# Optimization experiments

Hardware: AMD Instinct MI355X
Metric: run time of the kernel (lower is better)

Reference implementation:

```python
import jax, jax.numpy as jnp
import numpy as np

B, S, D = 8, 4096, 1024
G, V = 2, 320
TAU = 1.0
EPS = 1e-7


def setup_inputs() -> dict:
    key = jax.random.key(0)
    k_x, k_w, k_cb, k_u = jax.random.split(key, 4)
    x = jax.random.normal(k_x, (B, S, D), dtype=jnp.float32)
    W = jax.random.normal(k_w, (D, G * V), dtype=jnp.float32) * (1.0 / np.sqrt(D))
    b = jnp.zeros((G * V,), dtype=jnp.float32)
    # nn.init.uniform_ -> U(0,1); codebooks viewed as [G, V, D//G]
    codebooks = jax.random.uniform(k_cb, (G, V, D // G), dtype=jnp.float32)
    # standard Gumbel(0,1) noise, one per logit: shape [B*S*G, V]
    u = jax.random.uniform(k_u, (B * S * G, V), dtype=jnp.float32,
                           minval=1e-6, maxval=1.0 - 1e-6)
    gumbel = -jnp.log(-jnp.log(u))
    return {"x": x, "W": W, "b": b, "codebooks": codebooks, "gumbel": gumbel}


def reference(x, W, b, codebooks, gumbel):
    Bx, Sx, Dx = x.shape
    Gx, Vx, _ = codebooks.shape
    N = Bx * Sx
    # logit projection: [B,S,D] @ [D, G*V] -> flatten to [N*G, V]
    logits = (jnp.einsum('bsd,de->bse', x, W) + b).reshape(N * Gx, Vx)
    # gumbel-softmax, hard=True with straight-through estimator
    y_soft = jax.nn.softmax((logits + gumbel) / TAU, axis=-1)
    idx = jnp.argmax(y_soft, axis=-1)
    y_hard = jax.nn.one_hot(idx, Vx, dtype=y_soft.dtype)
    one_hot_st = y_hard + y_soft - jax.lax.stop_gradient(y_soft)  # fwd == y_hard
    # codebook lookup via (mostly one-hot) contraction: [N,G,V] x [G,V,d] -> [N,G,d]
    q = jnp.einsum('ngv,gvd->ngd', one_hot_st.reshape(N, Gx, Vx), codebooks)
    quantized = q.reshape(Bx, Sx, Dx)
    # perplexity from clean (non-gumbel) softmax probs
    probs = jax.nn.softmax(logits.reshape(N, Gx, Vx), axis=-1)
    avg_probs = probs.mean(axis=0)  # [G, V]
    perplexity = jnp.exp(-jnp.sum(avg_probs * jnp.log(avg_probs + EPS), axis=-1)).mean()
    return (quantized, perplexity)
```

## Files before the change

kernel.cpp:

```cpp
#include <hip/hip_runtime.h>
#include <hip/hip_bf16.h>
#include <math.h>

#define NROWS 32768
#define DD    1024
#define EE    640
#define VV    320
#define BM    64
#define KT    32
#define CTN   40

typedef __attribute__((ext_vector_type(8))) short short8;
typedef __attribute__((ext_vector_type(4))) short short4v;
typedef __attribute__((ext_vector_type(4))) float float4v;

static __device__ __forceinline__ unsigned short f2bf(float f) {
    unsigned int u = __float_as_uint(f);
    return (unsigned short)((u + 0x7fffu + ((u >> 16) & 1u)) >> 16);
}

static __device__ __forceinline__ void gload_lds16(const void* g, void* l) {
    __builtin_amdgcn_global_load_lds(
        (const __attribute__((address_space(1))) unsigned int*)g,
        (__attribute__((address_space(3))) unsigned int*)l, 16, 0, 0);
}

__global__ void pack_w(const float* __restrict__ W, unsigned short* __restrict__ bp)
{
    const int t = threadIdx.x;
    const int tile = blockIdx.x * 4 + (t >> 6);
    const int lane = t & 63;
    const int kt = tile / CTN, ct = tile % CTN;
    const int k0 = kt * 32 + (lane >> 4) * 8;
    const int col = ct * 16 + (lane & 15);
    unsigned short v1[8];
    #pragma unroll
    for (int e = 0; e < 8; ++e)
        v1[e] = f2bf(W[(size_t)(k0 + e) * EE + col]);
    *(short8*)(bp + ((size_t)tile * 64 + lane) * 8) = *(const short8*)v1;
}

__global__ __launch_bounds__(512, 4) void fused_mfma(
    const float* __restrict__ x, const unsigned short* __restrict__ bp,
    const float* __restrict__ bias, const float* __restrict__ cb,
    const float* __restrict__ gum, float* __restrict__ out,
    float* __restrict__ probs_acc)
{
    __shared__ unsigned short Bs[32 * EE];
    __shared__ unsigned short As[BM * 32];
    __shared__ float probs_blk[EE];
    __shared__ float pmax[8][BM];
    __shared__ float psum[8][BM];
    __shared__ int   pidx[8][BM];
    __shared__ int   fidx[BM][2];
    __shared__ float finv[BM][2];

    const int t    = threadIdx.x;
    const int lane = t & 63;
    const int cg   = t >> 6;
    const int n0   = blockIdx.x * BM;

    float4v acc[4][5];
    #pragma unroll
    for (int rf = 0; rf < 4; ++rf)
        #pragma unroll
        for (int ct = 0; ct < 5; ++ct)
            acc[rf][ct] = (float4v)0.f;

    const int r0 = t >> 3, kq0 = t & 7;
    const int abase = (r0 >> 4)*512 + ((r0 & 15) + ((kq0 >> 1) << 4))*8 + ((kq0 & 1) << 2);
    const float* xr = x + (size_t)(n0 + r0) * DD + kq0 * 4;

    auto writeA = [&](float4 v) {
        short4v s1;
        s1[0] = (short)f2bf(v.x); s1[1] = (short)f2bf(v.y);
        s1[2] = (short)f2bf(v.z); s1[3] = (short)f2bf(v.w);
        *(short4v*)&As[abase] = s1;
    };
    auto stageB = [&](int kt) {
        const unsigned short* src = bp + (size_t)kt * (32 * EE);
        #pragma unroll
        for (int s = 0; s < 5; ++s) {
            const int q = s * 512 + t;
            gload_lds16(src + (size_t)q * 8, &Bs[q * 8]);
        }
    };

    float4 pA = *(const float4*)(xr);
    stageB(0);
    __syncthreads();
    writeA(pA);
    __syncthreads();

    for (int kt = 0; kt < KT; ++kt) {
        const bool more = (kt + 1 < KT);
        if (more) pA = *(const float4*)(xr + (kt + 1) * 32);

        short8 af[4];
        #pragma unroll
        for (int rf = 0; rf < 4; ++rf)
            af[rf] = *(const short8*)&As[rf*512 + lane*8];
        #pragma unroll
        for (int ct = 0; ct < 5; ++ct) {
            short8 bf = *(const short8*)&Bs[((cg*5 + ct)*64 + lane)*8];
            #pragma unroll
            for (int rf = 0; rf < 4; ++rf)
                acc[rf][ct] = __builtin_amdgcn_mfma_f32_16x16x32_bf16(af[rf], bf, acc[rf][ct], 0, 0, 0);
        }
        __syncthreads();
        if (more) {
            stageB(kt + 1);
            writeA(pA);
        }
        __syncthreads();
    }

    {
        float bv[5];
        #pragma unroll
        for (int ct = 0; ct < 5; ++ct) bv[ct] = bias[cg*80 + ct*16 + (lane & 15)];
        #pragma unroll
        for (int rf = 0; rf < 4; ++rf)
            #pragma unroll
            for (int ct = 0; ct < 5; ++ct) {
                acc[rf][ct][0] += bv[ct]; acc[rf][ct][1] += bv[ct];
                acc[rf][ct][2] += bv[ct]; acc[rf][ct][3] += bv[ct];
            }
    }

    const int g = cg >> 2;
    const int goff0 = (cg & 3)*80 + (lane & 15);
    #pragma unroll
    for (int rf = 0; rf < 4; ++rf) {
        #pragma unroll
        for (int r = 0; r < 4; ++r) {
            const int rowA = rf*16 + ((lane >> 4) << 2) + r;
            const float* grow = gum + ((size_t)(n0 + rowA)*2 + g)*VV + goff0;
            float m1 = -1e30f; int bi = 0; float es = 0.f;
            #pragma unroll
            for (int ct = 0; ct < 5; ++ct) {
                float z  = acc[rf][ct][r];
                float zg = z + grow[ct*16];
                if (zg > m1) { m1 = zg; bi = goff0 + ct*16; }
                es += __expf(z);
            }
            #pragma unroll
            for (int off = 1; off < 16; off <<= 1) {
                float om = __shfl_xor(m1, off);
                int   ob = __shfl_xor(bi, off);
                if (om > m1 || (om == m1 && ob < bi)) { m1 = om; bi = ob; }
                es += __shfl_xor(es, off);
            }
            if ((lane & 15) == 0) {
                pmax[cg][rowA] = m1; pidx[cg][rowA] = bi; psum[cg][rowA] = es;
            }
        }
    }
    for (int c = t; c < EE; c += 512) probs_blk[c] = 0.f;
    __syncthreads();

    if (t < 128) {
        const int row = t & 63, gg = t >> 6;
        float m1 = -1e30f; int bi = 0x7fffffff; float s = 0.f;
        #pragma unroll
        for (int c = 0; c < 4; ++c) {
            const float om = pmax[gg*4 + c][row];
            const int   ob = pidx[gg*4 + c][row];
            if (om > m1 || (om == m1 && ob < bi)) { m1 = om; bi = ob; }
            s += psum[gg*4 + c][row];
        }
        fidx[row][gg] = bi;
        finv[row][gg] = 1.f / s;
    }
    __syncthreads();

    float pacc[5];
    #pragma unroll
    for (int ct = 0; ct < 5; ++ct) pacc[ct] = 0.f;
    #pragma unroll
    for (int rf = 0; rf < 4; ++rf) {
        #pragma unroll
        for (int r = 0; r < 4; ++r) {
            const int rowA = rf*16 + ((lane >> 4) << 2) + r;
            const float inv = finv[rowA][g];
            #pragma unroll
            for (int ct = 0; ct < 5; ++ct)
                pacc[ct] += __expf(acc[rf][ct][r]) * inv;
        }
    }
    #pragma unroll
    for (int off = 16; off < 64; off <<= 1)
        #pragma unroll
        for (int ct = 0; ct < 5; ++ct)
            pacc[ct] += __shfl_xor(pacc[ct], off);
    if (lane < 16) {
        #pragma unroll
        for (int ct = 0; ct < 5; ++ct)
            atomicAdd(&probs_blk[cg*80 + ct*16 + lane], pacc[ct]);
    }
    __syncthreads();

    for (int c = t; c < EE; c += 512)
        atomicAdd(&probs_acc[c], probs_blk[c]);

    for (int i = t; i < BM*256; i += 512) {
        const int row = i >> 8, f4 = i & 255;
        const int gg  = f4 >> 7;
        const int idx = fidx[row][gg];
        const float4 v = *(const float4*)&cb[((size_t)gg*VV + idx)*512 + (size_t)(f4 & 127)*4];
        *(float4*)&out[(size_t)(n0 + row)*DD + (size_t)f4*4] = v;
    }
}

__global__ void perp_kernel(const float* __restrict__ probs_acc,
                            float* __restrict__ outp)
{
    __shared__ float s0[4], s1[4];
    int t = threadIdx.x;
    float p0 = 0.f, p1 = 0.f;
    for (int c = t; c < EE; c += 256) {
        float a = probs_acc[c] * (1.0f / NROWS);
        float v = a * logf(a + 1e-7f);
        if (c < VV) p0 += v; else p1 += v;
    }
    #pragma unroll
    for (int off = 1; off < 64; off <<= 1) {
        p0 += __shfl_xor(p0, off);
        p1 += __shfl_xor(p1, off);
    }
    if ((t & 63) == 0) { s0[t >> 6] = p0; s1[t >> 6] = p1; }
    __syncthreads();
    if (t == 0) {
        float a0 = s0[0] + s0[1] + s0[2] + s0[3];
        float a1 = s1[0] + s1[1] + s1[2] + s1[3];
        outp[0] = 0.5f * (expf(-a0) + expf(-a1));
    }
}

extern "C" void kernel_launch(void* const* d_in, const int* in_sizes, int n_in,
                              void* d_out, int out_size, void* d_ws, size_t ws_size,
                              hipStream_t stream)
{
    const float* x   = (const float*)d_in[0];
    const float* W   = (const float*)d_in[1];
    const float* b   = (const float*)d_in[2];
    const float* cb  = (const float*)d_in[3];
    const float* gum = (const float*)d_in[4];
    float* out = (float*)d_out;

    unsigned short* bp = (unsigned short*)d_ws;
    float* probs_acc = (float*)((char*)d_ws + (size_t)DD*EE*2);

    hipMemsetAsync(probs_acc, 0, EE * sizeof(float), stream);
    pack_w<<<320, 256, 0, stream>>>(W, bp);
    fused_mfma<<<NROWS / BM, 512, 0, stream>>>(x, bp, b, cb, gum, out, probs_acc);
    perp_kernel<<<1, 256, 0, stream>>>(probs_acc, out + (out_size - 1));
}
```

Before: 131.0 us.

## Double-buffer LDS tiles and double row tile to 1024-thread blocks

The row tile per block grows from 64 to 128, so each W tile staged into LDS now serves twice as many rows, using 16 waves arranged as 2 row groups by 8 column groups. The A and B LDS tiles are double-buffered: the next K-step's global-to-LDS copy is issued before the current MFMA work, which drops one barrier per iteration. The cost is roughly 100 KB of LDS per block, so only one block fits per CU. The launch bound of (1024, 4) may also squeeze the register budget hard enough to cause spills of the 80-float accumulator array.

```diff
diff --git a/kernel.cpp b/kernel.cpp
--- a/kernel.cpp
+++ b/kernel.cpp
@@ -6,7 +6,7 @@
 #define DD    1024
 #define EE    640
 #define VV    320
-#define BM    64
+#define BM    128
 #define KT    32
 #define CTN   40
 
@@ -40,14 +40,14 @@
     *(short8*)(bp + ((size_t)tile * 64 + lane) * 8) = *(const short8*)v1;
 }
 
-__global__ __launch_bounds__(512, 4) void fused_mfma(
+__global__ __launch_bounds__(1024, 4) void fused_mfma(
     const float* __restrict__ x, const unsigned short* __restrict__ bp,
     const float* __restrict__ bias, const float* __restrict__ cb,
     const float* __restrict__ gum, float* __restrict__ out,
     float* __restrict__ probs_acc)
 {
-    __shared__ unsigned short Bs[32 * EE];
-    __shared__ unsigned short As[BM * 32];
+    __shared__ unsigned short Bs[2][32 * EE];
+    __shared__ unsigned short As[2][BM * 32];
     __shared__ float probs_blk[EE];
     __shared__ float pmax[8][BM];
     __shared__ float psum[8][BM];
@@ -57,7 +57,9 @@
 
     const int t    = threadIdx.x;
     const int lane = t & 63;
-    const int cg   = t >> 6;
+    const int w    = t >> 6;
+    const int rg   = w >> 3;
+    const int cg   = w & 7;
     const int n0   = blockIdx.x * BM;
 
     float4v acc[4][5];
@@ -71,48 +73,47 @@
     const int abase = (r0 >> 4)*512 + ((r0 & 15) + ((kq0 >> 1) << 4))*8 + ((kq0 & 1) << 2);
     const float* xr = x + (size_t)(n0 + r0) * DD + kq0 * 4;
 
-    auto writeA = [&](float4 v) {
+    auto writeA = [&](int bb, float4 v) {
         short4v s1;
         s1[0] = (short)f2bf(v.x); s1[1] = (short)f2bf(v.y);
         s1[2] = (short)f2bf(v.z); s1[3] = (short)f2bf(v.w);
-        *(short4v*)&As[abase] = s1;
+        *(short4v*)&As[bb][abase] = s1;
     };
-    auto stageB = [&](int kt) {
+    auto stageB = [&](int bb, int kt) {
         const unsigned short* src = bp + (size_t)kt * (32 * EE);
-        #pragma unroll
-        for (int s = 0; s < 5; ++s) {
-            const int q = s * 512 + t;
-            gload_lds16(src + (size_t)q * 8, &Bs[q * 8]);
-        }
+        gload_lds16(src + (size_t)t * 8,          &Bs[bb][t * 8]);
+        gload_lds16(src + (size_t)(t + 1024) * 8, &Bs[bb][(t + 1024) * 8]);
+        if (t < 512)
+            gload_lds16(src + (size_t)(t + 2048) * 8, &Bs[bb][(t + 2048) * 8]);
     };
 
     float4 pA = *(const float4*)(xr);
-    stageB(0);
-    __syncthreads();
-    writeA(pA);
-    __syncthreads();
-
+    stageB(0, 0);
+    __syncthreads();
+    writeA(0, pA);
+    __syncthreads();
+
+    int cur = 0;
     for (int kt = 0; kt < KT; ++kt) {
         const bool more = (kt + 1 < KT);
-        if (more) pA = *(const float4*)(xr + (kt + 1) * 32);
-
+        if (more) {
+            stageB(cur ^ 1, kt + 1);
+            pA = *(const float4*)(xr + (kt + 1) * 32);
+        }
         short8 af[4];
         #pragma unroll
         for (int rf = 0; rf < 4; ++rf)
-            af[rf] = *(const short8*)&As[rf*512 + lane*8];
+            af[rf] = *(const short8*)&As[cur][(rg*4 + rf)*512 + lane*8];
         #pragma unroll
         for (int ct = 0; ct < 5; ++ct) {
-            short8 bf = *(const short8*)&Bs[((cg*5 + ct)*64 + lane)*8];
+            short8 bf = *(const short8*)&Bs[cur][((cg*5 + ct)*64 + lane)*8];
             #pragma unroll
             for (int rf = 0; rf < 4; ++rf)
                 acc[rf][ct] = __builtin_amdgcn_mfma_f32_16x16x32_bf16(af[rf], bf, acc[rf][ct], 0, 0, 0);
         }
+        if (more) writeA(cur ^ 1, pA);
         __syncthreads();
-        if (more) {
-            stageB(kt + 1);
-            writeA(pA);
-        }
-        __syncthreads();
+        cur ^= 1;
     }
 
     {
@@ -134,7 +135,7 @@
     for (int rf = 0; rf < 4; ++rf) {
         #pragma unroll
         for (int r = 0; r < 4; ++r) {
-            const int rowA = rf*16 + ((lane >> 4) << 2) + r;
+            const int rowA = rg*64 + rf*16 + ((lane >> 4) << 2) + r;
             const float* grow = gum + ((size_t)(n0 + rowA)*2 + g)*VV + goff0;
             float m1 = -1e30f; int bi = 0; float es = 0.f;
             #pragma unroll
@@ -156,11 +157,11 @@
             }
         }
     }
-    for (int c = t; c < EE; c += 512) probs_blk[c] = 0.f;
-    __syncthreads();
-
-    if (t < 128) {
-        const int row = t & 63, gg = t >> 6;
+    for (int c = t; c < EE; c += 1024) probs_blk[c] = 0.f;
+    __syncthreads();
+
+    if (t < 256) {
+        const int row = t & 127, gg = t >> 7;
         float m1 = -1e30f; int bi = 0x7fffffff; float s = 0.f;
         #pragma unroll
         for (int c = 0; c < 4; ++c) {
@@ -181,7 +182,7 @@
     for (int rf = 0; rf < 4; ++rf) {
         #pragma unroll
         for (int r = 0; r < 4; ++r) {
-            const int rowA = rf*16 + ((lane >> 4) << 2) + r;
+            const int rowA = rg*64 + rf*16 + ((lane >> 4) << 2) + r;
             const float inv = finv[rowA][g];
             #pragma unroll
             for (int ct = 0; ct < 5; ++ct)
@@ -200,10 +201,10 @@
     }
     __syncthreads();
 
-    for (int c = t; c < EE; c += 512)
+    for (int c = t; c < EE; c += 1024)
         atomicAdd(&probs_acc[c], probs_blk[c]);
 
-    for (int i = t; i < BM*256; i += 512) {
+    for (int i = t; i < BM*256; i += 1024) {
         const int row = i >> 8, f4 = i & 255;
         const int gg  = f4 >> 7;
         const int idx = fidx[row][gg];
@@ -253,6 +254,6 @@
 
     hipMemsetAsync(probs_acc, 0, EE * sizeof(float), stream);
     pack_w<<<320, 256, 0, stream>>>(W, bp);
-    fused_mfma<<<NROWS / BM, 512, 0, stream>>>(x, bp, b, cb, gum, out, probs_acc);
+    fused_mfma<<<NROWS / BM, 1024, 0, stream>>>(x, bp, b, cb, gum, out, probs_acc);
     perp_kernel<<<1, 256, 0, stream>>>(probs_acc, out + (out_size - 1));
 }
```

New measurement: 130.6 us. Within noise of the previous version (-0.3%).

## Split fused kernel into GEMM writing bf16 logits and separate epilogue kernel

Applied to the files above, without the earlier changes.

Unfuses the projection from the softmax/argmax/codebook epilogue. The GEMM now stores bias-added logits as bf16 to workspace, double-buffers B tiles in LDS, and loads A directly from global with in-register bf16 conversion instead of staging through LDS. A new epilogue kernel processes 16 rows per block using LDS copies of logits and gumbel noise. Probability sums are accumulated into 8 replicated buffers to reduce atomic contention. This adds a logits round trip through memory and bf16 rounding of logits before argmax, and every wave now loads the same A data redundantly.

```diff
diff --git a/kernel.cpp b/kernel.cpp
--- a/kernel.cpp
+++ b/kernel.cpp
@@ -6,19 +6,28 @@
 #define DD    1024
 #define EE    640
 #define VV    320
-#define BM    64
 #define KT    32
 #define CTN   40
 
 typedef __attribute__((ext_vector_type(8))) short short8;
-typedef __attribute__((ext_vector_type(4))) short short4v;
 typedef __attribute__((ext_vector_type(4))) float float4v;
 
 static __device__ __forceinline__ unsigned short f2bf(float f) {
     unsigned int u = __float_as_uint(f);
     return (unsigned short)((u + 0x7fffu + ((u >> 16) & 1u)) >> 16);
 }
-
+static __device__ __forceinline__ float bf2f(unsigned short h) {
+    return __uint_as_float(((unsigned int)h) << 16);
+}
+static __device__ __forceinline__ short8 cvt8(float4 a, float4 b) {
+    float2 f0 = {a.x, a.y}, f1 = {a.z, a.w}, f2 = {b.x, b.y}, f3 = {b.z, b.w};
+    union { __hip_bfloat162 h[4]; short8 s; } u;
+    u.h[0] = __float22bfloat162_rn(f0);
+    u.h[1] = __float22bfloat162_rn(f1);
+    u.h[2] = __float22bfloat162_rn(f2);
+    u.h[3] = __float22bfloat162_rn(f3);
+    return u.s;
+}
 static __device__ __forceinline__ void gload_lds16(const void* g, void* l) {
     __builtin_amdgcn_global_load_lds(
         (const __attribute__((address_space(1))) unsigned int*)g,
@@ -40,25 +49,16 @@
     *(short8*)(bp + ((size_t)tile * 64 + lane) * 8) = *(const short8*)v1;
 }
 
-__global__ __launch_bounds__(512, 4) void fused_mfma(
+__global__ __launch_bounds__(512, 4) void gemm_z2(
     const float* __restrict__ x, const unsigned short* __restrict__ bp,
-    const float* __restrict__ bias, const float* __restrict__ cb,
-    const float* __restrict__ gum, float* __restrict__ out,
-    float* __restrict__ probs_acc)
-{
-    __shared__ unsigned short Bs[32 * EE];
-    __shared__ unsigned short As[BM * 32];
-    __shared__ float probs_blk[EE];
-    __shared__ float pmax[8][BM];
-    __shared__ float psum[8][BM];
-    __shared__ int   pidx[8][BM];
-    __shared__ int   fidx[BM][2];
-    __shared__ float finv[BM][2];
+    const float* __restrict__ bias, unsigned short* __restrict__ z)
+{
+    __shared__ unsigned short Bs[2][32 * EE];
 
     const int t    = threadIdx.x;
     const int lane = t & 63;
     const int cg   = t >> 6;
-    const int n0   = blockIdx.x * BM;
+    const int n0   = blockIdx.x * 64;
 
     float4v acc[4][5];
     #pragma unroll
@@ -67,159 +67,147 @@
         for (int ct = 0; ct < 5; ++ct)
             acc[rf][ct] = (float4v)0.f;
 
-    const int r0 = t >> 3, kq0 = t & 7;
-    const int abase = (r0 >> 4)*512 + ((r0 & 15) + ((kq0 >> 1) << 4))*8 + ((kq0 & 1) << 2);
-    const float* xr = x + (size_t)(n0 + r0) * DD + kq0 * 4;
-
-    auto writeA = [&](float4 v) {
-        short4v s1;
-        s1[0] = (short)f2bf(v.x); s1[1] = (short)f2bf(v.y);
-        s1[2] = (short)f2bf(v.z); s1[3] = (short)f2bf(v.w);
-        *(short4v*)&As[abase] = s1;
-    };
-    auto stageB = [&](int kt) {
+    const float* xl = x + (size_t)(n0 + (lane & 15)) * DD + (lane >> 4) * 8;
+
+    auto stageB = [&](int bb, int kt) {
         const unsigned short* src = bp + (size_t)kt * (32 * EE);
         #pragma unroll
         for (int s = 0; s < 5; ++s) {
             const int q = s * 512 + t;
-            gload_lds16(src + (size_t)q * 8, &Bs[q * 8]);
+            gload_lds16(src + (size_t)q * 8, &Bs[bb][q * 8]);
         }
     };
 
-    float4 pA = *(const float4*)(xr);
-    stageB(0);
-    __syncthreads();
-    writeA(pA);
-    __syncthreads();
-
+    stageB(0, 0);
     for (int kt = 0; kt < KT; ++kt) {
-        const bool more = (kt + 1 < KT);
-        if (more) pA = *(const float4*)(xr + (kt + 1) * 32);
+        asm volatile("s_waitcnt vmcnt(0)" ::: "memory");
+        __builtin_amdgcn_s_barrier();
+        __builtin_amdgcn_sched_barrier(0);
+        if (kt + 1 < KT) stageB((kt + 1) & 1, kt + 1);
+        __builtin_amdgcn_sched_barrier(0);
 
         short8 af[4];
         #pragma unroll
-        for (int rf = 0; rf < 4; ++rf)
-            af[rf] = *(const short8*)&As[rf*512 + lane*8];
+        for (int rf = 0; rf < 4; ++rf) {
+            float4 a0 = *(const float4*)(xl + (size_t)rf * 16 * DD + kt * 32);
+            float4 a1 = *(const float4*)(xl + (size_t)rf * 16 * DD + kt * 32 + 4);
+            af[rf] = cvt8(a0, a1);
+        }
         #pragma unroll
         for (int ct = 0; ct < 5; ++ct) {
-            short8 bf = *(const short8*)&Bs[((cg*5 + ct)*64 + lane)*8];
+            short8 bf = *(const short8*)&Bs[kt & 1][((cg*5 + ct)*64 + lane)*8];
             #pragma unroll
             for (int rf = 0; rf < 4; ++rf)
                 acc[rf][ct] = __builtin_amdgcn_mfma_f32_16x16x32_bf16(af[rf], bf, acc[rf][ct], 0, 0, 0);
         }
-        __syncthreads();
-        if (more) {
-            stageB(kt + 1);
-            writeA(pA);
-        }
-        __syncthreads();
-    }
+    }
+
+    float bv[5];
+    const int cb0 = cg * 80 + (lane & 15);
+    #pragma unroll
+    for (int ct = 0; ct < 5; ++ct) bv[ct] = bias[cb0 + ct*16];
+    #pragma unroll
+    for (int rf = 0; rf < 4; ++rf) {
+        #pragma unroll
+        for (int r = 0; r < 4; ++r) {
+            const size_t n = (size_t)(n0 + rf*16 + ((lane >> 4) << 2) + r);
+            #pragma unroll
+            for (int ct = 0; ct < 5; ++ct)
+                z[n*EE + cb0 + ct*16] = f2bf(acc[rf][ct][r] + bv[ct]);
+        }
+    }
+}
+
+__global__ __launch_bounds__(512, 2) void epi2(
+    const unsigned short* __restrict__ z, const float* __restrict__ gum,
+    const float* __restrict__ cb, float* __restrict__ out,
+    float* __restrict__ probs_rep)
+{
+    __shared__ unsigned short zs[16 * EE];
+    __shared__ float          gs[16 * EE];
+    __shared__ float inv[16][2];
+    __shared__ int   sidx[16][2];
+
+    const int t = threadIdx.x;
+    const size_t r0 = (size_t)blockIdx.x * 16;
 
     {
-        float bv[5];
-        #pragma unroll
-        for (int ct = 0; ct < 5; ++ct) bv[ct] = bias[cg*80 + ct*16 + (lane & 15)];
-        #pragma unroll
-        for (int rf = 0; rf < 4; ++rf)
-            #pragma unroll
-            for (int ct = 0; ct < 5; ++ct) {
-                acc[rf][ct][0] += bv[ct]; acc[rf][ct][1] += bv[ct];
-                acc[rf][ct][2] += bv[ct]; acc[rf][ct][3] += bv[ct];
-            }
-    }
-
-    const int g = cg >> 2;
-    const int goff0 = (cg & 3)*80 + (lane & 15);
-    #pragma unroll
-    for (int rf = 0; rf < 4; ++rf) {
-        #pragma unroll
-        for (int r = 0; r < 4; ++r) {
-            const int rowA = rf*16 + ((lane >> 4) << 2) + r;
-            const float* grow = gum + ((size_t)(n0 + rowA)*2 + g)*VV + goff0;
-            float m1 = -1e30f; int bi = 0; float es = 0.f;
-            #pragma unroll
-            for (int ct = 0; ct < 5; ++ct) {
-                float z  = acc[rf][ct][r];
-                float zg = z + grow[ct*16];
-                if (zg > m1) { m1 = zg; bi = goff0 + ct*16; }
-                es += __expf(z);
-            }
-            #pragma unroll
-            for (int off = 1; off < 16; off <<= 1) {
-                float om = __shfl_xor(m1, off);
-                int   ob = __shfl_xor(bi, off);
-                if (om > m1 || (om == m1 && ob < bi)) { m1 = om; bi = ob; }
-                es += __shfl_xor(es, off);
-            }
-            if ((lane & 15) == 0) {
-                pmax[cg][rowA] = m1; pidx[cg][rowA] = bi; psum[cg][rowA] = es;
-            }
-        }
-    }
-    for (int c = t; c < EE; c += 512) probs_blk[c] = 0.f;
+        const uint4* src = (const uint4*)(z + r0 * EE);
+        uint4* dst = (uint4*)zs;
+        dst[t]       = src[t];
+        dst[t + 512] = src[t + 512];
+        if (t < 256) dst[t + 1024] = src[t + 1024];
+        const uint4* gsrc = (const uint4*)(gum + r0 * 2 * VV);
+        uint4* gdst = (uint4*)gs;
+        #pragma unroll
+        for (int s = 0; s < 5; ++s) gdst[t + s*512] = gsrc[t + s*512];
+    }
     __syncthreads();
 
-    if (t < 128) {
-        const int row = t & 63, gg = t >> 6;
-        float m1 = -1e30f; int bi = 0x7fffffff; float s = 0.f;
-        #pragma unroll
-        for (int c = 0; c < 4; ++c) {
-            const float om = pmax[gg*4 + c][row];
-            const int   ob = pidx[gg*4 + c][row];
+    {
+        const int row = t >> 5, j = t & 31, g = j >> 4, vb = (j & 15) * 20;
+        const unsigned short* zrow = &zs[row * EE + g * VV + vb];
+        const float* grow = &gs[row * EE + g * VV + vb];
+        float m1 = -1e30f; int bi = 0; float es = 0.f;
+        #pragma unroll
+        for (int k = 0; k < 20; ++k) {
+            const float zj = bf2f(zrow[k]);
+            const float zg = zj + grow[k];
+            if (zg > m1) { m1 = zg; bi = vb + k; }
+            es += __expf(zj);
+        }
+        #pragma unroll
+        for (int off = 1; off < 16; off <<= 1) {
+            float om = __shfl_xor(m1, off);
+            int   ob = __shfl_xor(bi, off);
             if (om > m1 || (om == m1 && ob < bi)) { m1 = om; bi = ob; }
-            s += psum[gg*4 + c][row];
-        }
-        fidx[row][gg] = bi;
-        finv[row][gg] = 1.f / s;
+            es += __shfl_xor(es, off);
+        }
+        if ((j & 15) == 0) { sidx[row][g] = bi; inv[row][g] = 1.f / es; }
     }
     __syncthreads();
 
-    float pacc[5];
-    #pragma unroll
-    for (int ct = 0; ct < 5; ++ct) pacc[ct] = 0.f;
-    #pragma unroll
-    for (int rf = 0; rf < 4; ++rf) {
-        #pragma unroll
-        for (int r = 0; r < 4; ++r) {
-            const int rowA = rf*16 + ((lane >> 4) << 2) + r;
-            const float inv = finv[rowA][g];
-            #pragma unroll
-            for (int ct = 0; ct < 5; ++ct)
-                pacc[ct] += __expf(acc[rf][ct][r]) * inv;
-        }
-    }
-    #pragma unroll
-    for (int off = 16; off < 64; off <<= 1)
-        #pragma unroll
-        for (int ct = 0; ct < 5; ++ct)
-            pacc[ct] += __shfl_xor(pacc[ct], off);
-    if (lane < 16) {
-        #pragma unroll
-        for (int ct = 0; ct < 5; ++ct)
-            atomicAdd(&probs_blk[cg*80 + ct*16 + lane], pacc[ct]);
-    }
-    __syncthreads();
-
-    for (int c = t; c < EE; c += 512)
-        atomicAdd(&probs_acc[c], probs_blk[c]);
-
-    for (int i = t; i < BM*256; i += 512) {
-        const int row = i >> 8, f4 = i & 255;
-        const int gg  = f4 >> 7;
-        const int idx = fidx[row][gg];
+    {
+        const int rep = blockIdx.x & 7;
+        int c = t;
+        {
+            const int gg = (c >= VV);
+            float s = 0.f;
+            #pragma unroll
+            for (int rr = 0; rr < 16; ++rr)
+                s += __expf(bf2f(zs[rr * EE + c])) * inv[rr][gg];
+            atomicAdd(&probs_rep[rep * EE + c], s);
+        }
+        if (t < 128) {
+            c = 512 + t;
+            float s = 0.f;
+            #pragma unroll
+            for (int rr = 0; rr < 16; ++rr)
+                s += __expf(bf2f(zs[rr * EE + c])) * inv[rr][1];
+            atomicAdd(&probs_rep[rep * EE + c], s);
+        }
+    }
+
+    for (int i = t; i < 16 * 256; i += 512) {
+        const int rr = i >> 8, f4 = i & 255;
+        const int gg = f4 >> 7;
+        const int idx = sidx[rr][gg];
         const float4 v = *(const float4*)&cb[((size_t)gg*VV + idx)*512 + (size_t)(f4 & 127)*4];
-        *(float4*)&out[(size_t)(n0 + row)*DD + (size_t)f4*4] = v;
-    }
-}
-
-__global__ void perp_kernel(const float* __restrict__ probs_acc,
-                            float* __restrict__ outp)
+        *(float4*)&out[(r0 + rr)*DD + (size_t)f4*4] = v;
+    }
+}
+
+__global__ void perp8_kernel(const float* __restrict__ probs_rep,
+                             float* __restrict__ outp)
 {
     __shared__ float s0[4], s1[4];
     int t = threadIdx.x;
     float p0 = 0.f, p1 = 0.f;
     for (int c = t; c < EE; c += 256) {
-        float a = probs_acc[c] * (1.0f / NROWS);
+        float a = 0.f;
+        #pragma unroll
+        for (int rp = 0; rp < 8; ++rp) a += probs_rep[rp*EE + c];
+        a *= (1.0f / NROWS);
         float v = a * logf(a + 1e-7f);
         if (c < VV) p0 += v; else p1 += v;
     }
@@ -248,11 +236,16 @@
     const float* gum = (const float*)d_in[4];
     float* out = (float*)d_out;
 
-    unsigned short* bp = (unsigned short*)d_ws;
-    float* probs_acc = (float*)((char*)d_ws + (size_t)DD*EE*2);
-
-    hipMemsetAsync(probs_acc, 0, EE * sizeof(float), stream);
+    char* wsp = (char*)d_ws;
+    unsigned short* bp = (unsigned short*)wsp;
+    const size_t bp_b = (size_t)DD*EE*2;
+    float* probs_rep = (float*)(wsp + bp_b);
+    const size_t pr_b = 8*EE*sizeof(float);
+    unsigned short* z = (unsigned short*)(wsp + bp_b + pr_b);
+
+    hipMemsetAsync(probs_rep, 0, pr_b, stream);
     pack_w<<<320, 256, 0, stream>>>(W, bp);
-    fused_mfma<<<NROWS / BM, 512, 0, stream>>>(x, bp, b, cb, gum, out, probs_acc);
-    perp_kernel<<<1, 256, 0, stream>>>(probs_acc, out + (out_size - 1));
-}
+    gemm_z2<<<NROWS / 64, 512, 0, stream>>>(x, bp, b, z);
+    epi2<<<NROWS / 16, 512, 0, stream>>>(z, gum, cb, out, probs_rep);
+    perp8_kernel<<<1, 256, 0, stream>>>(probs_rep, out + (out_size - 1));
+}
```

Result: slower. 230.6 us (+76.0%).

## Switch logit GEMM to FP8 MFMA with double-buffered LDS staging

Applied to the files above, without the earlier changes.

Converts both the x tiles and the packed W (pre-scaled by 16) to FP8 and uses the fp8 16x16x32 MFMA, rescaling the accumulators before adding the bias. LDS buffers for A and B are double-buffered so the next tile's load is issued before the current MFMAs, which drops one barrier per k-step. The probability accumulation is spread across 8 replicated global buffers to reduce atomic contention, and the final kernel sums the replicas. FP8 precision can change argmax indices on near-ties and alter the perplexity, which risks accuracy.

```diff
diff --git a/kernel.cpp b/kernel.cpp
--- a/kernel.cpp
+++ b/kernel.cpp
@@ -10,14 +10,8 @@
 #define KT    32
 #define CTN   40
 
-typedef __attribute__((ext_vector_type(8))) short short8;
-typedef __attribute__((ext_vector_type(4))) short short4v;
 typedef __attribute__((ext_vector_type(4))) float float4v;
-
-static __device__ __forceinline__ unsigned short f2bf(float f) {
-    unsigned int u = __float_as_uint(f);
-    return (unsigned short)((u + 0x7fffu + ((u >> 16) & 1u)) >> 16);
-}
+typedef long long i64t;
 
 static __device__ __forceinline__ void gload_lds16(const void* g, void* l) {
     __builtin_amdgcn_global_load_lds(
@@ -25,7 +19,7 @@
         (__attribute__((address_space(3))) unsigned int*)l, 16, 0, 0);
 }
 
-__global__ void pack_w(const float* __restrict__ W, unsigned short* __restrict__ bp)
+__global__ void pack_w8(const float* __restrict__ W, unsigned char* __restrict__ bp)
 {
     const int t = threadIdx.x;
     const int tile = blockIdx.x * 4 + (t >> 6);
@@ -33,21 +27,27 @@
     const int kt = tile / CTN, ct = tile % CTN;
     const int k0 = kt * 32 + (lane >> 4) * 8;
     const int col = ct * 16 + (lane & 15);
-    unsigned short v1[8];
+    float v[8];
     #pragma unroll
     for (int e = 0; e < 8; ++e)
-        v1[e] = f2bf(W[(size_t)(k0 + e) * EE + col]);
-    *(short8*)(bp + ((size_t)tile * 64 + lane) * 8) = *(const short8*)v1;
-}
-
-__global__ __launch_bounds__(512, 4) void fused_mfma(
-    const float* __restrict__ x, const unsigned short* __restrict__ bp,
+        v[e] = 16.0f * W[(size_t)(k0 + e) * EE + col];
+    int lo = 0, hi = 0;
+    lo = __builtin_amdgcn_cvt_pk_fp8_f32(v[0], v[1], lo, false);
+    lo = __builtin_amdgcn_cvt_pk_fp8_f32(v[2], v[3], lo, true);
+    hi = __builtin_amdgcn_cvt_pk_fp8_f32(v[4], v[5], hi, false);
+    hi = __builtin_amdgcn_cvt_pk_fp8_f32(v[6], v[7], hi, true);
+    int2 pk; pk.x = lo; pk.y = hi;
+    *(int2*)(bp + ((size_t)tile * 64 + lane) * 8) = pk;
+}
+
+__global__ __launch_bounds__(512, 4) void fused_vq(
+    const float* __restrict__ x, const unsigned char* __restrict__ bp,
     const float* __restrict__ bias, const float* __restrict__ cb,
     const float* __restrict__ gum, float* __restrict__ out,
-    float* __restrict__ probs_acc)
-{
-    __shared__ unsigned short Bs[32 * EE];
-    __shared__ unsigned short As[BM * 32];
+    float* __restrict__ probs_rep)
+{
+    __shared__ unsigned char Bs[2][32 * EE];
+    __shared__ unsigned char As[2][BM * 32];
     __shared__ float probs_blk[EE];
     __shared__ float pmax[8][BM];
     __shared__ float psum[8][BM];
@@ -71,47 +71,45 @@
     const int abase = (r0 >> 4)*512 + ((r0 & 15) + ((kq0 >> 1) << 4))*8 + ((kq0 & 1) << 2);
     const float* xr = x + (size_t)(n0 + r0) * DD + kq0 * 4;
 
-    auto writeA = [&](float4 v) {
-        short4v s1;
-        s1[0] = (short)f2bf(v.x); s1[1] = (short)f2bf(v.y);
-        s1[2] = (short)f2bf(v.z); s1[3] = (short)f2bf(v.w);
-        *(short4v*)&As[abase] = s1;
+    auto writeA = [&](int bb, float4 v) {
+        int pk = 0;
+        pk = __builtin_amdgcn_cvt_pk_fp8_f32(v.x, v.y, pk, false);
+        pk = __builtin_amdgcn_cvt_pk_fp8_f32(v.z, v.w, pk, true);
+        *(int*)&As[bb][abase] = pk;
     };
-    auto stageB = [&](int kt) {
-        const unsigned short* src = bp + (size_t)kt * (32 * EE);
-        #pragma unroll
-        for (int s = 0; s < 5; ++s) {
-            const int q = s * 512 + t;
-            gload_lds16(src + (size_t)q * 8, &Bs[q * 8]);
-        }
+    auto stageB = [&](int bb, int kt) {
+        const unsigned char* src = bp + (size_t)kt * (32 * EE);
+        gload_lds16(src + (size_t)t * 16,          &Bs[bb][t * 16]);
+        gload_lds16(src + (size_t)(t + 512) * 16,  &Bs[bb][(t + 512) * 16]);
+        if (t < 256)
+            gload_lds16(src + (size_t)(t + 1024) * 16, &Bs[bb][(t + 1024) * 16]);
     };
 
     float4 pA = *(const float4*)(xr);
-    stageB(0);
-    __syncthreads();
-    writeA(pA);
+    stageB(0, 0);
+    __syncthreads();
+    writeA(0, pA);
     __syncthreads();
 
     for (int kt = 0; kt < KT; ++kt) {
+        const int bb = kt & 1;
         const bool more = (kt + 1 < KT);
-        if (more) pA = *(const float4*)(xr + (kt + 1) * 32);
-
-        short8 af[4];
+        if (more) {
+            stageB(bb ^ 1, kt + 1);
+            pA = *(const float4*)(xr + (kt + 1) * 32);
+        }
+        i64t af[4];
         #pragma unroll
         for (int rf = 0; rf < 4; ++rf)
-            af[rf] = *(const short8*)&As[rf*512 + lane*8];
+            af[rf] = *(const i64t*)&As[bb][rf*512 + lane*8];
         #pragma unroll
         for (int ct = 0; ct < 5; ++ct) {
-            short8 bf = *(const short8*)&Bs[((cg*5 + ct)*64 + lane)*8];
+            i64t bf = *(const i64t*)&Bs[bb][((cg*5 + ct)*64 + lane)*8];
             #pragma unroll
             for (int rf = 0; rf < 4; ++rf)
-                acc[rf][ct] = __builtin_amdgcn_mfma_f32_16x16x32_bf16(af[rf], bf, acc[rf][ct], 0, 0, 0);
-        }
-        __syncthreads();
-        if (more) {
-            stageB(kt + 1);
-            writeA(pA);
-        }
+                acc[rf][ct] = __builtin_amdgcn_mfma_f32_16x16x32_fp8_fp8(af[rf], bf, acc[rf][ct], 0, 0, 0);
+        }
+        if (more) writeA(bb ^ 1, pA);
         __syncthreads();
     }
 
@@ -122,10 +120,10 @@
         #pragma unroll
         for (int rf = 0; rf < 4; ++rf)
             #pragma unroll
-            for (int ct = 0; ct < 5; ++ct) {
-                acc[rf][ct][0] += bv[ct]; acc[rf][ct][1] += bv[ct];
-                acc[rf][ct][2] += bv[ct]; acc[rf][ct][3] += bv[ct];
-            }
+            for (int ct = 0; ct < 5; ++ct)
+                #pragma unroll
+                for (int r = 0; r < 4; ++r)
+                    acc[rf][ct][r] = acc[rf][ct][r] * 0.0625f + bv[ct];
     }
 
     const int g = cg >> 2;
@@ -139,10 +137,10 @@
             float m1 = -1e30f; int bi = 0; float es = 0.f;
             #pragma unroll
             for (int ct = 0; ct < 5; ++ct) {
-                float z  = acc[rf][ct][r];
-                float zg = z + grow[ct*16];
+                float zv = acc[rf][ct][r];
+                float zg = zv + grow[ct*16];
                 if (zg > m1) { m1 = zg; bi = goff0 + ct*16; }
-                es += __expf(z);
+                es += __expf(zv);
             }
             #pragma unroll
             for (int off = 1; off < 16; off <<= 1) {
@@ -200,8 +198,9 @@
     }
     __syncthreads();
 
+    const int rep = blockIdx.x & 7;
     for (int c = t; c < EE; c += 512)
-        atomicAdd(&probs_acc[c], probs_blk[c]);
+        atomicAdd(&probs_rep[rep*EE + c], probs_blk[c]);
 
     for (int i = t; i < BM*256; i += 512) {
         const int row = i >> 8, f4 = i & 255;
@@ -212,14 +211,17 @@
     }
 }
 
-__global__ void perp_kernel(const float* __restrict__ probs_acc,
-                            float* __restrict__ outp)
+__global__ void perp8_kernel(const float* __restrict__ probs_rep,
+                             float* __restrict__ outp)
 {
     __shared__ float s0[4], s1[4];
     int t = threadIdx.x;
     float p0 = 0.f, p1 = 0.f;
     for (int c = t; c < EE; c += 256) {
-        float a = probs_acc[c] * (1.0f / NROWS);
+        float a = 0.f;
+        #pragma unroll
+        for (int rp = 0; rp < 8; ++rp) a += probs_rep[rp*EE + c];
+        a *= (1.0f / NROWS);
         float v = a * logf(a + 1e-7f);
         if (c < VV) p0 += v; else p1 += v;
     }
@@ -248,11 +250,14 @@
     const float* gum = (const float*)d_in[4];
     float* out = (float*)d_out;
 
-    unsigned short* bp = (unsigned short*)d_ws;
-    float* probs_acc = (float*)((char*)d_ws + (size_t)DD*EE*2);
-
-    hipMemsetAsync(probs_acc, 0, EE * sizeof(float), stream);
-    pack_w<<<320, 256, 0, stream>>>(W, bp);
-    fused_mfma<<<NROWS / BM, 512, 0, stream>>>(x, bp, b, cb, gum, out, probs_acc);
-    perp_kernel<<<1, 256, 0, stream>>>(probs_acc, out + (out_size - 1));
-}
+    char* wsp = (char*)d_ws;
+    unsigned char* bp = (unsigned char*)wsp;
+    const size_t bp_b = (size_t)DD*EE;
+    float* probs_rep = (float*)(wsp + bp_b);
+    const size_t pr_b = 8*EE*sizeof(float);
+
+    hipMemsetAsync(probs_rep, 0, pr_b, stream);
+    pack_w8<<<320, 256, 0, stream>>>(W, bp);
+    fused_vq<<<NROWS / BM, 512, 0, stream>>>(x, bp, b, cb, gum, out, probs_rep);
+    perp8_kernel<<<1, 256, 0, stream>>>(probs_rep, out + (out_size - 1));
+}
```

Measured after the change: 116.8 us, median of 2. 1.12x faster.
